# Performance work log

Measured on AMD Instinct MI355X. Metric: run time of the kernel, lower is better.

Reference implementation:

```python
import jax, jax.numpy as jnp
import numpy as np

ALPHA = 1.0  # module hardcodes self.alpha = 1.0


def _normalize(m):
    # torch: diag(rowsum^-0.5) @ m @ diag(rowsum^-0.5) == broadcast row/col scaling
    r_inv = jnp.sum(m, axis=0) ** -0.5  # [V]
    return m * r_inv[:, None] * r_inv[None, :]


def setup_inputs() -> dict:
    key = jax.random.key(0)
    k1, k2, k3, k4 = jax.random.split(key, 4)
    V, D_IN, D_OUT, A, B = 2048, 64, 64, 8, 8
    adj = jax.random.uniform(k1, (V, V), dtype=jnp.float32)
    x = jax.random.normal(k2, (A, B, V, D_IN), dtype=jnp.float32)
    # xavier_normal_ on [D_IN, D_OUT]
    std = float(np.sqrt(2.0 / (D_IN + D_OUT)))
    weight = jax.random.normal(k3, (D_IN, D_OUT), dtype=jnp.float32) * std
    bias = jax.random.normal(k4, (D_OUT,), dtype=jnp.float32)
    return {"adj": adj, "x": x, "weight": weight, "bias": bias}


def reference(adj, x, weight, bias):
    # dropout is identity in eval mode
    adj_norm = _normalize(adj)
    sqr_norm = _normalize(adj @ adj)  # computed as in the original (alpha=1 zeroes it)
    m_norm = ALPHA * adj_norm + (1.0 - ALPHA) * sqr_norm  # [V, V]
    x_tmp = jnp.einsum('abvd,de->abve', x, weight)        # project features
    x_out = jnp.einsum('vj,abvd->abjd', m_norm, x_tmp)    # aggregate over nodes
    x_out = x_out + bias
    return jax.nn.relu(x_out)
```

## Files before the change

### kernel.cpp

```cpp
#include <hip/hip_runtime.h>
#include <cstddef>

typedef unsigned short u16;
typedef u16 u16x8 __attribute__((ext_vector_type(8)));
typedef __bf16 bf16x8 __attribute__((ext_vector_type(8)));
typedef float f32x4 __attribute__((ext_vector_type(4)));

static constexpr int V  = 2048;
static constexpr int DD = 64;

__device__ __forceinline__ u16 f2b(float f) {
  union { float f; unsigned int i; } x; x.f = f;
  return (u16)((x.i + 0x7fffu + ((x.i >> 16) & 1u)) >> 16);
}

__device__ __forceinline__ void gll16(const void* g, void* l) {
  __builtin_amdgcn_global_load_lds(
      (const __attribute__((address_space(1))) void*)g,
      (__attribute__((address_space(3))) void*)l, 16, 0, 0);
}

__global__ __launch_bounds__(256) void k_part(const float* __restrict__ adj,
                                              float* __restrict__ partial) {
  int t = threadIdx.x;
  int r0 = blockIdx.x * 32;
  int c0 = t * 8;
  float acc[8] = {0.f, 0.f, 0.f, 0.f, 0.f, 0.f, 0.f, 0.f};
  for (int r = 0; r < 32; ++r) {
    const float4* p = (const float4*)(adj + (size_t)(r0 + r) * V + c0);
    float4 a0 = p[0], a1 = p[1];
    acc[0] += a0.x; acc[1] += a0.y; acc[2] += a0.z; acc[3] += a0.w;
    acc[4] += a1.x; acc[5] += a1.y; acc[6] += a1.z; acc[7] += a1.w;
  }
  #pragma unroll
  for (int k = 0; k < 8; ++k) partial[(size_t)blockIdx.x * V + c0 + k] = acc[k];
}

__global__ __launch_bounds__(256) void k_prep(const float* __restrict__ adj,
                                              const float* __restrict__ partial,
                                              const float* __restrict__ x,
                                              const float* __restrict__ w,
                                              u16* __restrict__ At,
                                              u16* __restrict__ Yt) {
  __shared__ float T[64][65];
  __shared__ float rvv[64], rvj[64];
  int t = threadIdx.x;
  int bid = blockIdx.x;

  if (bid < 1024) {
    int v0 = (bid & 31) * 64;
    int j0 = (bid >> 5) * 64;
    if (t < 128) {
      int col = (t < 64) ? (v0 + t) : (j0 + (t - 64));
      float s = 0.f;
      for (int i = 0; i < 64; ++i) s += partial[(size_t)i * V + col];
      float rv = rsqrtf(s);
      if (t < 64) rvv[t] = rv; else rvj[t - 64] = rv;
    }
    __syncthreads();
    #pragma unroll
    for (int it = 0; it < 2; ++it) {
      int f = t + it * 256;
      int row = f >> 3;
      int cc = (f & 7) * 8;
      float rv = rvv[row];
      const float4* p = (const float4*)(adj + (size_t)(v0 + row) * V + j0 + cc);
      float4 a0 = p[0], a1 = p[1];
      T[row][cc + 0] = a0.x * rv; T[row][cc + 1] = a0.y * rv;
      T[row][cc + 2] = a0.z * rv; T[row][cc + 3] = a0.w * rv;
      T[row][cc + 4] = a1.x * rv; T[row][cc + 5] = a1.y * rv;
      T[row][cc + 6] = a1.z * rv; T[row][cc + 7] = a1.w * rv;
    }
    __syncthreads();
    #pragma unroll
    for (int it = 0; it < 2; ++it) {
      int f = t + it * 256;
      int jr = f >> 3;
      int vc = (f & 7) * 8;
      float rj = rvj[jr];
      u16x8 o;
      #pragma unroll
      for (int k = 0; k < 8; ++k) o[k] = f2b(T[vc + k][jr] * rj);
      *(u16x8*)(At + (size_t)(j0 + jr) * V + v0 + vc) = o;
    }
  } else {
    int pb = bid - 1024;
    int ab = pb >> 4;
    int v0 = (pb & 15) * 128;
    u16* WT = (u16*)&T[0][0];

    {
      const float4* pw = (const float4*)(w + t * 16);
      float4 c0 = pw[0], c1 = pw[1], c2 = pw[2], c3 = pw[3];
      float vals[16] = {c0.x, c0.y, c0.z, c0.w, c1.x, c1.y, c1.z, c1.w,
                        c2.x, c2.y, c2.z, c2.w, c3.x, c3.y, c3.z, c3.w};
      #pragma unroll
      for (int k = 0; k < 16; ++k) {
        int idx = t * 16 + k;
        WT[(idx & 63) * 72 + (idx >> 6)] = f2b(vals[k]);
      }
    }
    __syncthreads();

    int lane = t & 63, wave = t >> 6;
    int q = lane >> 4, r = lane & 15;
    int vbase = v0 + wave * 32;

    bf16x8 a[4][2];
    #pragma unroll
    for (int i = 0; i < 4; ++i)
      #pragma unroll
      for (int kk = 0; kk < 2; ++kk)
        a[i][kk] = __builtin_bit_cast(bf16x8,
            *(const u16x8*)(WT + (i * 16 + r) * 72 + kk * 32 + q * 8));

    const f32x4 vzero = {0.f, 0.f, 0.f, 0.f};
    f32x4 acc[4][2];
    #pragma unroll
    for (int i = 0; i < 4; ++i) { acc[i][0] = vzero; acc[i][1] = vzero; }

    #pragma unroll
    for (int nt = 0; nt < 2; ++nt) {
      int v = vbase + nt * 16 + r;
      const float* xp = x + ((size_t)ab * V + v) * DD;
      #pragma unroll
      for (int kk = 0; kk < 2; ++kk) {
        const float4* p = (const float4*)(xp + kk * 32 + q * 8);
        float4 b0 = p[0], b1 = p[1];
        u16x8 bu;
        bu[0] = f2b(b0.x); bu[1] = f2b(b0.y); bu[2] = f2b(b0.z); bu[3] = f2b(b0.w);
        bu[4] = f2b(b1.x); bu[5] = f2b(b1.y); bu[6] = f2b(b1.z); bu[7] = f2b(b1.w);
        bf16x8 bf = __builtin_bit_cast(bf16x8, bu);
        #pragma unroll
        for (int i = 0; i < 4; ++i)
          acc[i][nt] = __builtin_amdgcn_mfma_f32_16x16x32_bf16(a[i][kk], bf, acc[i][nt], 0, 0, 0);
      }
    }

    #pragma unroll
    for (int i = 0; i < 4; ++i)
      #pragma unroll
      for (int nt = 0; nt < 2; ++nt) {
        int v = vbase + nt * 16 + r;
        #pragma unroll
        for (int reg = 0; reg < 4; ++reg) {
          int e = i * 16 + q * 4 + reg;
          Yt[(size_t)(ab * 64 + e) * V + v] = f2b(acc[i][nt][reg]);
        }
      }
  }
}

static constexpr int ABUF  = 128 * 64;
static constexpr int BUFSZ = 2 * ABUF;

__global__ __launch_bounds__(256) void k_gemm(const u16* __restrict__ At,
                                              const u16* __restrict__ Yt,
                                              const float* __restrict__ bias,
                                              float* __restrict__ out) {
  __shared__ u16 lds[2 * BUFSZ];
  const int t = threadIdx.x;
  const int bid = blockIdx.x;
  const int swz = (bid & 7) * 64 + (bid >> 3);
  const int m0 = (swz & 15) * 128;
  const int n0 = (swz >> 4) * 128;
  const int lane = t & 63, wave = t >> 6;
  const int wm = (wave & 1) * 64;
  const int wn = (wave >> 1) * 64;
  const int q = lane >> 4, r = lane & 15;

  auto stage = [&](int base, int k0) {
    #pragma unroll
    for (int l = 0; l < 4; ++l) {
      int g = l * 256 + t;
      int row = g >> 3;
      int ch = (g & 7) ^ (row & 7);
      gll16(At + (size_t)(m0 + row) * V + k0 + ch * 8, (void*)(lds + base + g * 8));
      gll16(Yt + (size_t)(n0 + row) * V + k0 + ch * 8, (void*)(lds + base + ABUF + g * 8));
    }
  };

  const f32x4 vzero = {0.f, 0.f, 0.f, 0.f};
  f32x4 acc[4][4];
  #pragma unroll
  for (int i = 0; i < 4; ++i)
    #pragma unroll
    for (int j = 0; j < 4; ++j) acc[i][j] = vzero;

  stage(0, 0);
  asm volatile("s_waitcnt vmcnt(0)" ::: "memory");
  __builtin_amdgcn_s_barrier();

  int cb = 0;
  for (int tt = 0; tt < 32; ++tt) {
    const int nb = cb ^ BUFSZ;
    if (tt < 31) stage(nb, (tt + 1) * 64);
    __builtin_amdgcn_sched_barrier(0);

    #pragma unroll
    for (int kk = 0; kk < 2; ++kk) {
      bf16x8 a[4], b[4];
      #pragma unroll
      for (int i = 0; i < 4; ++i) {
        int row = wm + i * 16 + r;
        int c = (kk * 4 + q) ^ (row & 7);
        a[i] = __builtin_bit_cast(bf16x8,
            *(const u16x8*)(lds + cb + row * 64 + c * 8));
      }
      #pragma unroll
      for (int j = 0; j < 4; ++j) {
        int row = wn + j * 16 + r;
        int c = (kk * 4 + q) ^ (row & 7);
        b[j] = __builtin_bit_cast(bf16x8,
            *(const u16x8*)(lds + cb + ABUF + row * 64 + c * 8));
      }
      __builtin_amdgcn_s_setprio(1);
      #pragma unroll
      for (int i = 0; i < 4; ++i)
        #pragma unroll
        for (int j = 0; j < 4; ++j)
          acc[i][j] = __builtin_amdgcn_mfma_f32_16x16x32_bf16(
              a[i], b[j], acc[i][j], 0, 0, 0);
      __builtin_amdgcn_s_setprio(0);
    }

    asm volatile("s_waitcnt vmcnt(0)" ::: "memory");
    __builtin_amdgcn_s_barrier();
    cb = nb;
  }

  #pragma unroll
  for (int j = 0; j < 4; ++j) {
    int n = n0 + wn + j * 16 + r;
    int e = n & 63;
    int ab = n >> 6;
    float bv = bias[e];
    float* ob = out + (size_t)ab * (V * DD);
    #pragma unroll
    for (int i = 0; i < 4; ++i) {
      #pragma unroll
      for (int reg = 0; reg < 4; ++reg) {
        int jj = m0 + wm + i * 16 + q * 4 + reg;
        ob[(size_t)jj * DD + e] = fmaxf(acc[i][j][reg] + bv, 0.f);
      }
    }
  }
}

extern "C" void kernel_launch(void* const* d_in, const int* in_sizes, int n_in,
                              void* d_out, int out_size, void* d_ws, size_t ws_size,
                              hipStream_t stream) {
  const float* adj  = (const float*)d_in[0];
  const float* x    = (const float*)d_in[1];
  const float* w    = (const float*)d_in[2];
  const float* bias = (const float*)d_in[3];
  float* out = (float*)d_out;

  char* ws = (char*)d_ws;
  u16*   At      = (u16*)ws;
  u16*   Yt      = (u16*)(ws + ((size_t)8 << 20));
  float* partial = (float*)(ws + ((size_t)24 << 20));

  k_part<<<64, 256, 0, stream>>>(adj, partial);
  k_prep<<<2048, 256, 0, stream>>>(adj, partial, x, w, At, Yt);
  k_gemm<<<512, 256, 0, stream>>>(At, Yt, bias, out);
}
```

Before: 142.5 us.

## Run column-sum partials concurrently with feature projection, split normalize-transpose kernel

The standalone 64-block column-sum kernel is merged into a combined kernel whose first 256 blocks compute 32 row-group partial sums while the remaining blocks do the x@W projection. The normalize-and-transpose of adj becomes its own kernel that sums 32 partials per column instead of 64. This is meant to replace a poorly parallelized serial reduction launch with work that overlaps the projection and fills more of the GPU. The cost is that the adjacency transpose can no longer overlap with the projection.

```diff
diff --git a/kernel.cpp b/kernel.cpp
--- a/kernel.cpp
+++ b/kernel.cpp
@@ -20,74 +20,26 @@
       (__attribute__((address_space(3))) void*)l, 16, 0, 0);
 }
 
-__global__ __launch_bounds__(256) void k_part(const float* __restrict__ adj,
-                                              float* __restrict__ partial) {
-  int t = threadIdx.x;
-  int r0 = blockIdx.x * 32;
-  int c0 = t * 8;
-  float acc[8] = {0.f, 0.f, 0.f, 0.f, 0.f, 0.f, 0.f, 0.f};
-  for (int r = 0; r < 32; ++r) {
-    const float4* p = (const float4*)(adj + (size_t)(r0 + r) * V + c0);
-    float4 a0 = p[0], a1 = p[1];
-    acc[0] += a0.x; acc[1] += a0.y; acc[2] += a0.z; acc[3] += a0.w;
-    acc[4] += a1.x; acc[5] += a1.y; acc[6] += a1.z; acc[7] += a1.w;
-  }
-  #pragma unroll
-  for (int k = 0; k < 8; ++k) partial[(size_t)blockIdx.x * V + c0 + k] = acc[k];
-}
-
-__global__ __launch_bounds__(256) void k_prep(const float* __restrict__ adj,
-                                              const float* __restrict__ partial,
-                                              const float* __restrict__ x,
-                                              const float* __restrict__ w,
-                                              u16* __restrict__ At,
-                                              u16* __restrict__ Yt) {
-  __shared__ float T[64][65];
-  __shared__ float rvv[64], rvj[64];
+__global__ __launch_bounds__(256) void k_pp(const float* __restrict__ adj,
+                                            const float* __restrict__ x,
+                                            const float* __restrict__ w,
+                                            float* __restrict__ partial,
+                                            u16* __restrict__ Yt) {
+  __shared__ u16 WT[64 * 72];
   int t = threadIdx.x;
   int bid = blockIdx.x;
 
-  if (bid < 1024) {
-    int v0 = (bid & 31) * 64;
-    int j0 = (bid >> 5) * 64;
-    if (t < 128) {
-      int col = (t < 64) ? (v0 + t) : (j0 + (t - 64));
-      float s = 0.f;
-      for (int i = 0; i < 64; ++i) s += partial[(size_t)i * V + col];
-      float rv = rsqrtf(s);
-      if (t < 64) rvv[t] = rv; else rvj[t - 64] = rv;
-    }
-    __syncthreads();
-    #pragma unroll
-    for (int it = 0; it < 2; ++it) {
-      int f = t + it * 256;
-      int row = f >> 3;
-      int cc = (f & 7) * 8;
-      float rv = rvv[row];
-      const float4* p = (const float4*)(adj + (size_t)(v0 + row) * V + j0 + cc);
-      float4 a0 = p[0], a1 = p[1];
-      T[row][cc + 0] = a0.x * rv; T[row][cc + 1] = a0.y * rv;
-      T[row][cc + 2] = a0.z * rv; T[row][cc + 3] = a0.w * rv;
-      T[row][cc + 4] = a1.x * rv; T[row][cc + 5] = a1.y * rv;
-      T[row][cc + 6] = a1.z * rv; T[row][cc + 7] = a1.w * rv;
-    }
-    __syncthreads();
-    #pragma unroll
-    for (int it = 0; it < 2; ++it) {
-      int f = t + it * 256;
-      int jr = f >> 3;
-      int vc = (f & 7) * 8;
-      float rj = rvj[jr];
-      u16x8 o;
-      #pragma unroll
-      for (int k = 0; k < 8; ++k) o[k] = f2b(T[vc + k][jr] * rj);
-      *(u16x8*)(At + (size_t)(j0 + jr) * V + v0 + vc) = o;
-    }
+  if (bid < 256) {
+    int rg = bid >> 3, cg = bid & 7;
+    int col = cg * 256 + t;
+    const float* p = adj + (size_t)(rg * 64) * V + col;
+    float s = 0.f;
+    for (int r = 0; r < 64; ++r) s += p[(size_t)r * V];
+    partial[(size_t)rg * V + col] = s;
   } else {
-    int pb = bid - 1024;
+    int pb = bid - 256;
     int ab = pb >> 4;
     int v0 = (pb & 15) * 128;
-    u16* WT = (u16*)&T[0][0];
 
     {
       const float4* pw = (const float4*)(w + t * 16);
@@ -148,6 +100,52 @@
           Yt[(size_t)(ab * 64 + e) * V + v] = f2b(acc[i][nt][reg]);
         }
       }
+  }
+}
+
+__global__ __launch_bounds__(256) void k_tn(const float* __restrict__ adj,
+                                            const float* __restrict__ partial,
+                                            u16* __restrict__ At) {
+  __shared__ float T[64][65];
+  __shared__ float rvv[64], rvj[64];
+  int t = threadIdx.x;
+  int bid = blockIdx.x;
+  int v0 = (bid & 31) * 64;
+  int j0 = (bid >> 5) * 64;
+
+  if (t < 128) {
+    int col = (t < 64) ? (v0 + t) : (j0 + (t - 64));
+    float s = 0.f;
+    #pragma unroll
+    for (int i = 0; i < 32; ++i) s += partial[(size_t)i * V + col];
+    float rv = rsqrtf(s);
+    if (t < 64) rvv[t] = rv; else rvj[t - 64] = rv;
+  }
+  __syncthreads();
+  #pragma unroll
+  for (int it = 0; it < 2; ++it) {
+    int f = t + it * 256;
+    int row = f >> 3;
+    int cc = (f & 7) * 8;
+    float rv = rvv[row];
+    const float4* p = (const float4*)(adj + (size_t)(v0 + row) * V + j0 + cc);
+    float4 a0 = p[0], a1 = p[1];
+    T[row][cc + 0] = a0.x * rv; T[row][cc + 1] = a0.y * rv;
+    T[row][cc + 2] = a0.z * rv; T[row][cc + 3] = a0.w * rv;
+    T[row][cc + 4] = a1.x * rv; T[row][cc + 5] = a1.y * rv;
+    T[row][cc + 6] = a1.z * rv; T[row][cc + 7] = a1.w * rv;
+  }
+  __syncthreads();
+  #pragma unroll
+  for (int it = 0; it < 2; ++it) {
+    int f = t + it * 256;
+    int jr = f >> 3;
+    int vc = (f & 7) * 8;
+    float rj = rvj[jr];
+    u16x8 o;
+    #pragma unroll
+    for (int k = 0; k < 8; ++k) o[k] = f2b(T[vc + k][jr] * rj);
+    *(u16x8*)(At + (size_t)(j0 + jr) * V + v0 + vc) = o;
   }
 }
 
@@ -261,7 +259,7 @@
   u16*   Yt      = (u16*)(ws + ((size_t)8 << 20));
   float* partial = (float*)(ws + ((size_t)24 << 20));
 
-  k_part<<<64, 256, 0, stream>>>(adj, partial);
-  k_prep<<<2048, 256, 0, stream>>>(adj, partial, x, w, At, Yt);
+  k_pp<<<1280, 256, 0, stream>>>(adj, x, w, partial, Yt);
+  k_tn<<<1024, 256, 0, stream>>>(adj, partial, At);
   k_gemm<<<512, 256, 0, stream>>>(At, Yt, bias, out);
 }
```

After: 141.1 us, median of 2. Within noise of the previous version (-1.0%).
